# Optimization experiments

Hardware: AMD Instinct MI355X
Metric: run time of the kernel (lower is better)

Reference implementation:

```python
import jax, jax.numpy as jnp
import numpy as np

N_NODES = 100_000
N_EDGES = 1_250_000
IN_FEATS, N_HIDDEN, N_CLASSES = 64, 64, 32


def setup_inputs() -> dict:
    key = jax.random.key(0)
    ks = jax.random.split(key, 8)
    x = jax.random.normal(ks[0], (N_NODES, IN_FEATS), dtype=jnp.float32)
    src = jax.random.randint(ks[1], (N_EDGES,), 0, N_NODES, dtype=jnp.int64)
    dst = jax.random.randint(ks[2], (N_EDGES,), 0, N_NODES, dtype=jnp.int64)
    s1 = 1.0 / np.sqrt(IN_FEATS)
    s2 = 1.0 / np.sqrt(N_HIDDEN)
    W_self1 = jax.random.normal(ks[3], (IN_FEATS, N_HIDDEN), dtype=jnp.float32) * s1
    W_neigh1 = jax.random.normal(ks[4], (IN_FEATS, N_HIDDEN), dtype=jnp.float32) * s1
    b1 = jnp.zeros((N_HIDDEN,), dtype=jnp.float32)
    W_self2 = jax.random.normal(ks[5], (N_HIDDEN, N_CLASSES), dtype=jnp.float32) * s2
    W_neigh2 = jax.random.normal(ks[6], (N_HIDDEN, N_CLASSES), dtype=jnp.float32) * s2
    b2 = jnp.zeros((N_CLASSES,), dtype=jnp.float32)
    return dict(x=x, src=src, dst=dst, W_self1=W_self1, W_neigh1=W_neigh1, b1=b1,
                W_self2=W_self2, W_neigh2=W_neigh2, b2=b2)


def _sage_conv(h, src, dst, W_self, W_neigh, b):
    # mean aggregation over in-neighbors: gather src feats, segment-sum by dst
    n = h.shape[0]
    msg = h[src]  # [E, d] -- dominant memory traffic
    agg = jax.ops.segment_sum(msg, dst, num_segments=n)
    deg = jax.ops.segment_sum(jnp.ones_like(dst, dtype=h.dtype), dst, num_segments=n)
    h_neigh = agg / jnp.maximum(deg, 1.0)[:, None]  # zero-degree nodes get 0 (DGL behavior)
    return h @ W_self + h_neigh @ W_neigh + b


def reference(x, src, dst, W_self1, W_neigh1, b1, W_self2, W_neigh2, b2):
    h = _sage_conv(x, src, dst, W_self1, W_neigh1, b1)
    h = jax.nn.relu(h)
    # dropout(p=0.5) is identity in eval mode
    return _sage_conv(h, src, dst, W_self2, W_neigh2, b2)
```

## Files before the change

kernel.cpp:

```cpp
#include <hip/hip_runtime.h>
#include <hip/hip_bf16.h>


#define NF 64
#define BW 256
#define BSH 8
#define MAXB 512
#define CAPMAX 8192
#define P1_CHUNK 2048
#define H1S 68

typedef __attribute__((ext_vector_type(8))) short short8;
typedef __attribute__((ext_vector_type(8))) unsigned short ushort8v;
typedef __attribute__((ext_vector_type(4))) float floatx4;

__device__ __forceinline__ short bf16hi(float v) {
    __hip_bfloat16 h = __float2bfloat16(v);
    return *(short*)&h;
}
__device__ __forceinline__ float bf2f(short s) {
    __hip_bfloat16 h = *(__hip_bfloat16*)&s;
    return __bfloat162float(h);
}
__device__ __forceinline__ float bits2f(unsigned short u) {
    unsigned int x = ((unsigned int)u) << 16;
    union { unsigned int i; float f; } c; c.i = x; return c.f;
}


__global__ __launch_bounds__(512) void zero_kernel(int* __restrict__ g) {
    if (threadIdx.x < MAXB) g[threadIdx.x] = 0;
}


__global__ __launch_bounds__(256) void p1_bucket_kernel(const int* __restrict__ src,
                                                        const int* __restrict__ dst,
                                                        int* __restrict__ gcursor,
                                                        unsigned* __restrict__ bucket,
                                                        int E, int nbuckets) {
    __shared__ int cnt[MAXB];
    __shared__ int cbase[MAXB];
    const int beg = blockIdx.x * P1_CHUNK;
    const int end = min(E, beg + P1_CHUNK);
    for (int i = threadIdx.x; i < nbuckets; i += 256) cnt[i] = 0;
    __syncthreads();
    for (int e = beg + threadIdx.x; e < end; e += 256)
        atomicAdd(&cnt[dst[e] >> BSH], 1);
    __syncthreads();
    for (int i = threadIdx.x; i < nbuckets; i += 256) {
        int c = cnt[i];
        cbase[i] = c ? atomicAdd(&gcursor[i], c) : 0;
        cnt[i] = 0;
    }
    __syncthreads();
    for (int e = beg + threadIdx.x; e < end; e += 256) {
        int d = dst[e];
        int r = d >> BSH;
        int p = cbase[r] + atomicAdd(&cnt[r], 1);
        if (p < CAPMAX)
            bucket[(size_t)r * CAPMAX + p] = ((unsigned)src[e] << BSH) | (unsigned)(d & (BW - 1));
    }
}

__global__ __launch_bounds__(256) void p2_csr_kernel(const unsigned* __restrict__ bucket,
                                                     const int* __restrict__ gcursor,
                                                     int* __restrict__ row_start,
                                                     int* __restrict__ csr_src,
                                                     int N, int nbuckets) {
    __shared__ unsigned stage[CAPMAX];
    __shared__ int cnt[BW];
    __shared__ int excl[BW];
    const int r = blockIdx.x;
    const int tid = threadIdx.x;

    int partial = 0;
    for (int i = tid; i < r; i += 256) partial += min(gcursor[i], CAPMAX);
    excl[tid] = partial;
    __syncthreads();
    for (int off = 128; off > 0; off >>= 1) {
        if (tid < off) excl[tid] += excl[tid + off];
        __syncthreads();
    }
    const int base = excl[0];
    const int sz = min(gcursor[r], CAPMAX);
    const unsigned* bsrc = bucket + (size_t)r * CAPMAX;
    __syncthreads();

    cnt[tid] = 0;
    __syncthreads();
    for (int i = tid; i < sz; i += 256) {
        unsigned v = bsrc[i];
        stage[i] = v;
        atomicAdd(&cnt[v & (BW - 1)], 1);
    }
    __syncthreads();
    excl[tid] = cnt[tid];
    __syncthreads();
    for (int off = 1; off < BW; off <<= 1) {
        int v0 = (tid >= off) ? excl[tid - off] : 0;
        __syncthreads();
        excl[tid] += v0;
        __syncthreads();
    }
    int node = r * BW + tid;
    if (node < N) row_start[node] = base + excl[tid] - cnt[tid];
    if (r == nbuckets - 1 && tid == 0) row_start[N] = base + sz;
    __syncthreads();
    cnt[tid] = excl[tid] - cnt[tid];
    __syncthreads();
    for (int i = tid; i < sz; i += 256) {
        unsigned v = stage[i];
        int p = atomicAdd(&cnt[v & (BW - 1)], 1);
        csr_src[base + p] = (int)(v >> BSH);
    }
}


__global__ __launch_bounds__(256) void dense1_mfma_kernel(
        const float* __restrict__ X,
        const float* __restrict__ Wself,
        const float* __restrict__ Wneigh,
        const float* __restrict__ bias,
        float* __restrict__ outA,
        unsigned short* __restrict__ outB,
        int N) {
    constexpr int NT = 8, NSELF = 4, NO = 128, HALF = 64;
    __shared__ unsigned short wh[NO * 72];
    __shared__ unsigned short wl[NO * 72];
    const int tid = threadIdx.x;
    for (int i = tid; i < NO * 64; i += 256) {
        int n = i & (NO - 1), k = i / NO;
        float v = (n < HALF) ? Wself[k * HALF + n] : Wneigh[k * HALF + (n - HALF)];
        short hv = bf16hi(v);
        wh[n * 72 + k] = (unsigned short)hv;
        wl[n * 72 + k] = (unsigned short)bf16hi(v - bf2f(hv));
    }

    const int lane = tid & 63;
    const int wid  = tid >> 6;
    const int m = lane & 15, quad = lane >> 4;
    const int rowblk = blockIdx.x * 128 + wid * 32;

    floatx4 acc[2][NT];
    #pragma unroll
    for (int rt = 0; rt < 2; ++rt)
        #pragma unroll
        for (int t = 0; t < NT; ++t) acc[rt][t] = (floatx4)(0.f);

    short8 ah[2][2], al[2][2];
    #pragma unroll
    for (int rt = 0; rt < 2; ++rt) {
        int r = rowblk + rt * 16 + m;
        if (r >= N) r = N - 1;
        const float* xp = X + (size_t)r * 64 + quad * 8;
        #pragma unroll
        for (int h = 0; h < 2; ++h) {
            floatx4 f0 = *(const floatx4*)(xp + h * 32);
            floatx4 f1 = *(const floatx4*)(xp + h * 32 + 4);
            short8 hi, lo;
            #pragma unroll
            for (int j = 0; j < 4; ++j) {
                short hv = bf16hi(f0[j]);
                hi[j] = hv; lo[j] = bf16hi(f0[j] - bf2f(hv));
                short hv2 = bf16hi(f1[j]);
                hi[4 + j] = hv2; lo[4 + j] = bf16hi(f1[j] - bf2f(hv2));
            }
            ah[rt][h] = hi; al[rt][h] = lo;
        }
    }
    __syncthreads();

    #pragma unroll
    for (int t = 0; t < NT; ++t) {
        int n = t * 16 + m;
        const unsigned short* ph = wh + n * 72 + quad * 8;
        const unsigned short* pl = wl + n * 72 + quad * 8;
        #pragma unroll
        for (int h = 0; h < 2; ++h) {
            short8 bh = *(const short8*)(ph + h * 32);
            short8 bl = *(const short8*)(pl + h * 32);
            #pragma unroll
            for (int rt = 0; rt < 2; ++rt) {
                acc[rt][t] = __builtin_amdgcn_mfma_f32_16x16x32_bf16(ah[rt][h], bh, acc[rt][t], 0, 0, 0);
                acc[rt][t] = __builtin_amdgcn_mfma_f32_16x16x32_bf16(al[rt][h], bh, acc[rt][t], 0, 0, 0);
                acc[rt][t] = __builtin_amdgcn_mfma_f32_16x16x32_bf16(ah[rt][h], bl, acc[rt][t], 0, 0, 0);
            }
        }
    }

    #pragma unroll
    for (int rt = 0; rt < 2; ++rt) {
        #pragma unroll
        for (int t = 0; t < NT; ++t) {
            #pragma unroll
            for (int r4 = 0; r4 < 4; ++r4) {
                int row = rowblk + rt * 16 + quad * 4 + r4;
                if (row < N) {
                    if (t < NSELF) {
                        int col = t * 16 + m;
                        outA[(size_t)row * 64 + col] = acc[rt][t][r4] + bias[col];
                    } else {
                        int col = (t - NSELF) * 16 + m;
                        outB[(size_t)row * 64 + col] = (unsigned short)bf16hi(acc[rt][t][r4]);
                    }
                }
            }
        }
    }
}


__global__ __launch_bounds__(256) void agg64_d2_kernel(
        const unsigned short* __restrict__ t1n,
        const float* __restrict__ xs,
        const int* __restrict__ row_start,
        const int* __restrict__ csr_src,
        const float* __restrict__ Ws2,
        const float* __restrict__ Wn2,
        const float* __restrict__ b2,
        float* __restrict__ outD,
        unsigned short* __restrict__ t2n,
        int N) {
    __shared__ unsigned short w2h[64 * 72];
    __shared__ unsigned short w2l[64 * 72];
    __shared__ float h1s[16][H1S];
    const int tid = threadIdx.x;
    for (int i = tid; i < 64 * 64; i += 256) {
        int n = i & 63, k = i >> 6;
        float v = (n < 32) ? Ws2[k * 32 + n] : Wn2[k * 32 + (n - 32)];
        short hv = bf16hi(v);
        w2h[n * 72 + k] = (unsigned short)hv;
        w2l[n * 72 + k] = (unsigned short)bf16hi(v - bf2f(hv));
    }

    const int lane = tid & 63;
    const int wid  = tid >> 6;
    const int half = lane >> 5;
    const int g = (lane >> 3) & 3;
    const int c = lane & 7;
    const int nbase = blockIdx.x * 16;

    #pragma unroll
    for (int q = 0; q < 2; ++q) {
        const int ln = wid * 4 + q * 2 + half;
        const int n = nbase + ln;
        float acc[8] = {0.f, 0.f, 0.f, 0.f, 0.f, 0.f, 0.f, 0.f};
        int beg = 0, end = 0;
        if (n < N) { beg = row_start[n]; end = row_start[n + 1]; }
        for (int j = beg + g; j < end; j += 8) {
            int j2 = j + 4;
            int s0 = csr_src[j];
            ushort8v u0 = *(const ushort8v*)(t1n + (size_t)s0 * 64 + c * 8);
            if (j2 < end) {
                int s1 = csr_src[j2];
                ushort8v u1 = *(const ushort8v*)(t1n + (size_t)s1 * 64 + c * 8);
                #pragma unroll
                for (int i = 0; i < 8; ++i) acc[i] += bits2f(u0[i]) + bits2f(u1[i]);
            } else {
                #pragma unroll
                for (int i = 0; i < 8; ++i) acc[i] += bits2f(u0[i]);
            }
        }
        #pragma unroll
        for (int i = 0; i < 8; ++i) {
            float v = acc[i];
            v += __shfl_xor(v, 8);
            v += __shfl_xor(v, 16);
            acc[i] = v;
        }
        if (g == 0) {
            floatx4 h0, h1v;
            if (n < N) {
                float invd = 1.0f / fmaxf((float)(end - beg), 1.0f);
                size_t o = (size_t)n * 64 + c * 8;
                floatx4 x0 = *(const floatx4*)(xs + o);
                floatx4 x1 = *(const floatx4*)(xs + o + 4);
                #pragma unroll
                for (int i = 0; i < 4; ++i) {
                    h0[i]  = fmaxf(x0[i] + acc[i] * invd, 0.f);
                    h1v[i] = fmaxf(x1[i] + acc[4 + i] * invd, 0.f);
                }
            } else {
                h0 = (floatx4)(0.f); h1v = (floatx4)(0.f);
            }
            *(floatx4*)&h1s[ln][c * 8]     = h0;
            *(floatx4*)&h1s[ln][c * 8 + 4] = h1v;
        }
    }
    __syncthreads();

    const int m = lane & 15, quad = lane >> 4;
    short8 ah[2], al[2];
    #pragma unroll
    for (int h = 0; h < 2; ++h) {
        const float* hp = &h1s[m][quad * 8 + h * 32];
        floatx4 f0 = *(const floatx4*)hp;
        floatx4 f1 = *(const floatx4*)(hp + 4);
        short8 hi, lo;
        #pragma unroll
        for (int j = 0; j < 4; ++j) {
            short hv = bf16hi(f0[j]);
            hi[j] = hv; lo[j] = bf16hi(f0[j] - bf2f(hv));
            short hv2 = bf16hi(f1[j]);
            hi[4 + j] = hv2; lo[4 + j] = bf16hi(f1[j] - bf2f(hv2));
        }
        ah[h] = hi; al[h] = lo;
    }
    floatx4 acc2 = (floatx4)(0.f);
    const int coln = wid * 16 + m;
    const unsigned short* ph = w2h + coln * 72 + quad * 8;
    const unsigned short* pl = w2l + coln * 72 + quad * 8;
    #pragma unroll
    for (int h = 0; h < 2; ++h) {
        short8 bh = *(const short8*)(ph + h * 32);
        short8 bl = *(const short8*)(pl + h * 32);
        acc2 = __builtin_amdgcn_mfma_f32_16x16x32_bf16(ah[h], bh, acc2, 0, 0, 0);
        acc2 = __builtin_amdgcn_mfma_f32_16x16x32_bf16(al[h], bh, acc2, 0, 0, 0);
        acc2 = __builtin_amdgcn_mfma_f32_16x16x32_bf16(ah[h], bl, acc2, 0, 0, 0);
    }
    #pragma unroll
    for (int r4 = 0; r4 < 4; ++r4) {
        int node = nbase + quad * 4 + r4;
        if (node < N) {
            if (coln < 32) outD[(size_t)node * 32 + coln] = acc2[r4] + b2[coln];
            else t2n[(size_t)node * 32 + (coln - 32)] = (unsigned short)bf16hi(acc2[r4]);
        }
    }
}


__global__ __launch_bounds__(256) void agg32_kernel(float* io,
                                                    const unsigned short* __restrict__ t2n,
                                                    const int* __restrict__ row_start,
                                                    const int* __restrict__ csr_src, int N) {
    int n = (blockIdx.x * blockDim.x + threadIdx.x) >> 6;
    if (n >= N) return;
    int lane = threadIdx.x & 63;
    int g = lane >> 2, c = lane & 3;
    int beg = row_start[n], end = row_start[n + 1];
    float acc[8] = {0.f, 0.f, 0.f, 0.f, 0.f, 0.f, 0.f, 0.f};
    for (int j = beg + g; j < end; j += 32) {
        int j2 = j + 16;
        int s0 = csr_src[j];
        ushort8v u0 = *(const ushort8v*)(t2n + (size_t)s0 * 32 + c * 8);
        if (j2 < end) {
            int s1 = csr_src[j2];
            ushort8v u1 = *(const ushort8v*)(t2n + (size_t)s1 * 32 + c * 8);
            #pragma unroll
            for (int i = 0; i < 8; ++i) acc[i] += bits2f(u0[i]) + bits2f(u1[i]);
        } else {
            #pragma unroll
            for (int i = 0; i < 8; ++i) acc[i] += bits2f(u0[i]);
        }
    }
    #pragma unroll
    for (int i = 0; i < 8; ++i) {
        float v = acc[i];
        v += __shfl_xor(v, 4);
        v += __shfl_xor(v, 8);
        v += __shfl_xor(v, 16);
        v += __shfl_xor(v, 32);
        acc[i] = v;
    }
    if (g == 0) {
        float inv = 1.0f / fmaxf((float)(end - beg), 1.0f);
        size_t o = (size_t)n * 32 + c * 8;
        floatx4 s0 = *(const floatx4*)(io + o);
        floatx4 s1 = *(const floatx4*)(io + o + 4);
        floatx4 r0, r1;
        #pragma unroll
        for (int i = 0; i < 4; ++i) {
            r0[i] = s0[i] + acc[i] * inv;
            r1[i] = s1[i] + acc[4 + i] * inv;
        }
        *(floatx4*)(io + o) = r0;
        *(floatx4*)(io + o + 4) = r1;
    }
}


__global__ __launch_bounds__(256) void deg_kernel(const int* __restrict__ dst,
                                                  float* __restrict__ deg, int E) {
    int e = blockIdx.x * blockDim.x + threadIdx.x;
    if (e < E) atomicAdd(&deg[dst[e]], 1.0f);
}

__global__ __launch_bounds__(256) void agg_atomic_kernel(const float* __restrict__ feats,
                                                         const int* __restrict__ src,
                                                         const int* __restrict__ dst,
                                                         float* __restrict__ agg, int E) {
    int tid = blockIdx.x * blockDim.x + threadIdx.x;
    if (tid >= E * NF) return;
    int e = tid >> 6, f = tid & 63;
    atomicAdd(&agg[(size_t)dst[e] * NF + f], feats[(size_t)src[e] * NF + f]);
}

__global__ __launch_bounds__(256) void layer1_fb_kernel(const float* __restrict__ x,
                                                        const float* __restrict__ agg,
                                                        const float* __restrict__ deg,
                                                        const float* __restrict__ Wself,
                                                        const float* __restrict__ Wneigh,
                                                        const float* __restrict__ b,
                                                        float* __restrict__ h1, int N) {
    int tid = blockIdx.x * blockDim.x + threadIdx.x;
    if (tid >= N * NF) return;
    int n = tid >> 6, c = tid & 63;
    float inv = 1.0f / fmaxf(deg[n], 1.0f);
    const float* xrow = x + (size_t)n * NF;
    const float* arow = agg + (size_t)n * NF;
    float acc = b[c];
    #pragma unroll
    for (int k = 0; k < NF; ++k) {
        acc += xrow[k] * Wself[k * NF + c];
        acc += (arow[k] * inv) * Wneigh[k * NF + c];
    }
    h1[tid] = fmaxf(acc, 0.f);
}

__global__ __launch_bounds__(256) void layer2_fb_kernel(const float* __restrict__ h1,
                                                        const float* __restrict__ agg,
                                                        const float* __restrict__ deg,
                                                        const float* __restrict__ Wself,
                                                        const float* __restrict__ Wneigh,
                                                        const float* __restrict__ b,
                                                        float* __restrict__ out, int N) {
    int tid = blockIdx.x * blockDim.x + threadIdx.x;
    if (tid >= N * 32) return;
    int n = tid >> 5, c = tid & 31;
    float inv = 1.0f / fmaxf(deg[n], 1.0f);
    const float* hrow = h1 + (size_t)n * NF;
    const float* arow = agg + (size_t)n * NF;
    float acc = b[c];
    #pragma unroll
    for (int k = 0; k < NF; ++k) {
        acc += hrow[k] * Wself[k * 32 + c];
        acc += (arow[k] * inv) * Wneigh[k * 32 + c];
    }
    out[tid] = acc;
}


extern "C" void kernel_launch(void* const* d_in, const int* in_sizes, int n_in,
                              void* d_out, int out_size, void* d_ws, size_t ws_size,
                              hipStream_t stream) {
    const float* x        = (const float*)d_in[0];
    const int*   src      = (const int*)d_in[1];
    const int*   dst      = (const int*)d_in[2];
    const float* W_self1  = (const float*)d_in[3];
    const float* W_neigh1 = (const float*)d_in[4];
    const float* b1       = (const float*)d_in[5];
    const float* W_self2  = (const float*)d_in[6];
    const float* W_neigh2 = (const float*)d_in[7];
    const float* b2       = (const float*)d_in[8];
    float* out = (float*)d_out;

    const int N = in_sizes[0] / NF;
    const int E = in_sizes[1];
    const int nbuckets = (N + BW - 1) / BW;

    const size_t rsPad = ((size_t)N + 8) & ~7ull;
    int* gcursor   = (int*)d_ws;
    int* row_start = gcursor + MAXB;
    int* csr_src   = row_start + rsPad;
    uintptr_t pa = (uintptr_t)(csr_src + (((size_t)E + 7) & ~7ull));
    pa = (pa + 127) & ~(uintptr_t)127;
    float* bufA = (float*)pa;
    unsigned* bucket = (unsigned*)bufA;
    unsigned short* t1n = (unsigned short*)(bufA + (size_t)N * NF);
    unsigned short* t2n = t1n + (size_t)N * NF;
    size_t need = (size_t)((char*)(t2n + (size_t)N * 32) - (char*)d_ws);

    bool fast = ws_size >= need
             && nbuckets <= MAXB
             && (size_t)nbuckets * CAPMAX <= (size_t)N * NF
             && (size_t)E * 2 / (size_t)nbuckets <= CAPMAX
             && N < (1 << 24)
             && out_size >= N * 32;

    if (fast) {
        zero_kernel<<<1, 512, 0, stream>>>(gcursor);
        p1_bucket_kernel<<<(E + P1_CHUNK - 1) / P1_CHUNK, 256, 0, stream>>>(
            src, dst, gcursor, bucket, E, nbuckets);
        p2_csr_kernel<<<nbuckets, 256, 0, stream>>>(bucket, gcursor,
                                                    row_start, csr_src, N, nbuckets);
        int dblocks = (N + 127) / 128;
        dense1_mfma_kernel<<<dblocks, 256, 0, stream>>>(x, W_self1, W_neigh1, b1,
                                                        bufA, t1n, N);
        agg64_d2_kernel<<<(N + 15) / 16, 256, 0, stream>>>(
            t1n, bufA, row_start, csr_src, W_self2, W_neigh2, b2, out, t2n, N);
        agg32_kernel<<<(N * 64 + 255) / 256, 256, 0, stream>>>(out, t2n,
                                                               row_start, csr_src, N);
    } else {
        float* deg = (float*)d_ws;
        float* agg = deg + N;
        float* h1  = agg + (size_t)N * NF;
        hipMemsetAsync(deg, 0, (size_t)(N + (size_t)N * NF) * sizeof(float), stream);
        deg_kernel<<<(E + 255) / 256, 256, 0, stream>>>(dst, deg, E);
        int at = E * NF;
        agg_atomic_kernel<<<(at + 255) / 256, 256, 0, stream>>>(x, src, dst, agg, E);
        layer1_fb_kernel<<<(N * NF + 255) / 256, 256, 0, stream>>>(x, agg, deg, W_self1,
                                                                   W_neigh1, b1, h1, N);
        hipMemsetAsync(agg, 0, (size_t)N * NF * sizeof(float), stream);
        agg_atomic_kernel<<<(at + 255) / 256, 256, 0, stream>>>(h1, src, dst, agg, E);
        layer2_fb_kernel<<<(N * 32 + 255) / 256, 256, 0, stream>>>(h1, agg, deg, W_self2,
                                                                   W_neigh2, b2, out, N);
    }
}
```

Baseline: 226.5 us.

## Fuse edge bucketing and layer-1 dense GEMM into one launch

Merges the edge-bucketing pass and the first dense MFMA transform into a single kernel, with block IDs past the dense range running the bucketing work. The two independent stages can then share the GPU concurrently and one launch is saved. To avoid clobbering bufA, the bucket scratch moves to a separate workspace region after t2n when space allows, otherwise it falls back to sequential launches. The shared-memory footprint is now the larger of the two stage needs, which may lower occupancy for the bucketing blocks.

Result: faster. 215.3 us (median of 2 runs) (-4.9%).

```diff
diff --git a/kernel.cpp b/kernel.cpp
--- a/kernel.cpp
+++ b/kernel.cpp
@@ -33,90 +33,10 @@
 }
 
 
-__global__ __launch_bounds__(256) void p1_bucket_kernel(const int* __restrict__ src,
-                                                        const int* __restrict__ dst,
-                                                        int* __restrict__ gcursor,
-                                                        unsigned* __restrict__ bucket,
-                                                        int E, int nbuckets) {
-    __shared__ int cnt[MAXB];
-    __shared__ int cbase[MAXB];
-    const int beg = blockIdx.x * P1_CHUNK;
-    const int end = min(E, beg + P1_CHUNK);
-    for (int i = threadIdx.x; i < nbuckets; i += 256) cnt[i] = 0;
-    __syncthreads();
-    for (int e = beg + threadIdx.x; e < end; e += 256)
-        atomicAdd(&cnt[dst[e] >> BSH], 1);
-    __syncthreads();
-    for (int i = threadIdx.x; i < nbuckets; i += 256) {
-        int c = cnt[i];
-        cbase[i] = c ? atomicAdd(&gcursor[i], c) : 0;
-        cnt[i] = 0;
-    }
-    __syncthreads();
-    for (int e = beg + threadIdx.x; e < end; e += 256) {
-        int d = dst[e];
-        int r = d >> BSH;
-        int p = cbase[r] + atomicAdd(&cnt[r], 1);
-        if (p < CAPMAX)
-            bucket[(size_t)r * CAPMAX + p] = ((unsigned)src[e] << BSH) | (unsigned)(d & (BW - 1));
-    }
-}
-
-__global__ __launch_bounds__(256) void p2_csr_kernel(const unsigned* __restrict__ bucket,
-                                                     const int* __restrict__ gcursor,
-                                                     int* __restrict__ row_start,
-                                                     int* __restrict__ csr_src,
-                                                     int N, int nbuckets) {
-    __shared__ unsigned stage[CAPMAX];
-    __shared__ int cnt[BW];
-    __shared__ int excl[BW];
-    const int r = blockIdx.x;
-    const int tid = threadIdx.x;
-
-    int partial = 0;
-    for (int i = tid; i < r; i += 256) partial += min(gcursor[i], CAPMAX);
-    excl[tid] = partial;
-    __syncthreads();
-    for (int off = 128; off > 0; off >>= 1) {
-        if (tid < off) excl[tid] += excl[tid + off];
-        __syncthreads();
-    }
-    const int base = excl[0];
-    const int sz = min(gcursor[r], CAPMAX);
-    const unsigned* bsrc = bucket + (size_t)r * CAPMAX;
-    __syncthreads();
-
-    cnt[tid] = 0;
-    __syncthreads();
-    for (int i = tid; i < sz; i += 256) {
-        unsigned v = bsrc[i];
-        stage[i] = v;
-        atomicAdd(&cnt[v & (BW - 1)], 1);
-    }
-    __syncthreads();
-    excl[tid] = cnt[tid];
-    __syncthreads();
-    for (int off = 1; off < BW; off <<= 1) {
-        int v0 = (tid >= off) ? excl[tid - off] : 0;
-        __syncthreads();
-        excl[tid] += v0;
-        __syncthreads();
-    }
-    int node = r * BW + tid;
-    if (node < N) row_start[node] = base + excl[tid] - cnt[tid];
-    if (r == nbuckets - 1 && tid == 0) row_start[N] = base + sz;
-    __syncthreads();
-    cnt[tid] = excl[tid] - cnt[tid];
-    __syncthreads();
-    for (int i = tid; i < sz; i += 256) {
-        unsigned v = stage[i];
-        int p = atomicAdd(&cnt[v & (BW - 1)], 1);
-        csr_src[base + p] = (int)(v >> BSH);
-    }
-}
-
-
-__global__ __launch_bounds__(256) void dense1_mfma_kernel(
+__global__ __launch_bounds__(256) void p1_dense1_kernel(
+        const int* __restrict__ src, const int* __restrict__ dst,
+        int* __restrict__ gcursor, unsigned* __restrict__ bucket,
+        int E, int nbuckets, int dblocks,
         const float* __restrict__ X,
         const float* __restrict__ Wself,
         const float* __restrict__ Wneigh,
@@ -124,10 +44,39 @@
         float* __restrict__ outA,
         unsigned short* __restrict__ outB,
         int N) {
+    __shared__ int smem_i[9216];
+    const int tid = threadIdx.x;
+
+    if ((int)blockIdx.x >= dblocks) {
+        int* cnt   = smem_i;
+        int* cbase = smem_i + MAXB;
+        const int bid = blockIdx.x - dblocks;
+        const int beg = bid * P1_CHUNK;
+        const int end = min(E, beg + P1_CHUNK);
+        for (int i = tid; i < nbuckets; i += 256) cnt[i] = 0;
+        __syncthreads();
+        for (int e = beg + tid; e < end; e += 256)
+            atomicAdd(&cnt[dst[e] >> BSH], 1);
+        __syncthreads();
+        for (int i = tid; i < nbuckets; i += 256) {
+            int c = cnt[i];
+            cbase[i] = c ? atomicAdd(&gcursor[i], c) : 0;
+            cnt[i] = 0;
+        }
+        __syncthreads();
+        for (int e = beg + tid; e < end; e += 256) {
+            int d = dst[e];
+            int r = d >> BSH;
+            int p = cbase[r] + atomicAdd(&cnt[r], 1);
+            if (p < CAPMAX)
+                bucket[(size_t)r * CAPMAX + p] = ((unsigned)src[e] << BSH) | (unsigned)(d & (BW - 1));
+        }
+        return;
+    }
+
     constexpr int NT = 8, NSELF = 4, NO = 128, HALF = 64;
-    __shared__ unsigned short wh[NO * 72];
-    __shared__ unsigned short wl[NO * 72];
-    const int tid = threadIdx.x;
+    unsigned short* wh = (unsigned short*)smem_i;
+    unsigned short* wl = wh + NO * 72;
     for (int i = tid; i < NO * 64; i += 256) {
         int n = i & (NO - 1), k = i / NO;
         float v = (n < HALF) ? Wself[k * HALF + n] : Wneigh[k * HALF + (n - HALF)];
@@ -206,6 +155,60 @@
                 }
             }
         }
+    }
+}
+
+
+__global__ __launch_bounds__(256) void p2_csr_kernel(const unsigned* __restrict__ bucket,
+                                                     const int* __restrict__ gcursor,
+                                                     int* __restrict__ row_start,
+                                                     int* __restrict__ csr_src,
+                                                     int N, int nbuckets) {
+    __shared__ unsigned stage[CAPMAX];
+    __shared__ int cnt[BW];
+    __shared__ int excl[BW];
+    const int r = blockIdx.x;
+    const int tid = threadIdx.x;
+
+    int partial = 0;
+    for (int i = tid; i < r; i += 256) partial += min(gcursor[i], CAPMAX);
+    excl[tid] = partial;
+    __syncthreads();
+    for (int off = 128; off > 0; off >>= 1) {
+        if (tid < off) excl[tid] += excl[tid + off];
+        __syncthreads();
+    }
+    const int base = excl[0];
+    const int sz = min(gcursor[r], CAPMAX);
+    const unsigned* bsrc = bucket + (size_t)r * CAPMAX;
+    __syncthreads();
+
+    cnt[tid] = 0;
+    __syncthreads();
+    for (int i = tid; i < sz; i += 256) {
+        unsigned v = bsrc[i];
+        stage[i] = v;
+        atomicAdd(&cnt[v & (BW - 1)], 1);
+    }
+    __syncthreads();
+    excl[tid] = cnt[tid];
+    __syncthreads();
+    for (int off = 1; off < BW; off <<= 1) {
+        int v0 = (tid >= off) ? excl[tid - off] : 0;
+        __syncthreads();
+        excl[tid] += v0;
+        __syncthreads();
+    }
+    int node = r * BW + tid;
+    if (node < N) row_start[node] = base + excl[tid] - cnt[tid];
+    if (r == nbuckets - 1 && tid == 0) row_start[N] = base + sz;
+    __syncthreads();
+    cnt[tid] = excl[tid] - cnt[tid];
+    __syncthreads();
+    for (int i = tid; i < sz; i += 256) {
+        unsigned v = stage[i];
+        int p = atomicAdd(&cnt[v & (BW - 1)], 1);
+        csr_src[base + p] = (int)(v >> BSH);
     }
 }
 
@@ -479,13 +482,26 @@
 
     if (fast) {
         zero_kernel<<<1, 512, 0, stream>>>(gcursor);
-        p1_bucket_kernel<<<(E + P1_CHUNK - 1) / P1_CHUNK, 256, 0, stream>>>(
-            src, dst, gcursor, bucket, E, nbuckets);
-        p2_csr_kernel<<<nbuckets, 256, 0, stream>>>(bucket, gcursor,
-                                                    row_start, csr_src, N, nbuckets);
-        int dblocks = (N + 127) / 128;
-        dense1_mfma_kernel<<<dblocks, 256, 0, stream>>>(x, W_self1, W_neigh1, b1,
-                                                        bufA, t1n, N);
+        int dblocks  = (N + 127) / 128;
+        int p1blocks = (E + P1_CHUNK - 1) / P1_CHUNK;
+        unsigned* bucket2 = (unsigned*)(t2n + (((size_t)N * 32 + 63) & ~63ull));
+        size_t need2 = (size_t)((char*)(bucket2 + (size_t)nbuckets * CAPMAX) - (char*)d_ws);
+        if (ws_size >= need2) {
+            p1_dense1_kernel<<<dblocks + p1blocks, 256, 0, stream>>>(
+                src, dst, gcursor, bucket2, E, nbuckets, dblocks,
+                x, W_self1, W_neigh1, b1, bufA, t1n, N);
+            p2_csr_kernel<<<nbuckets, 256, 0, stream>>>(bucket2, gcursor,
+                                                        row_start, csr_src, N, nbuckets);
+        } else {
+            p1_dense1_kernel<<<p1blocks, 256, 0, stream>>>(
+                src, dst, gcursor, bucket, E, nbuckets, 0,
+                x, W_self1, W_neigh1, b1, bufA, t1n, N);
+            p2_csr_kernel<<<nbuckets, 256, 0, stream>>>(bucket, gcursor,
+                                                        row_start, csr_src, N, nbuckets);
+            p1_dense1_kernel<<<dblocks, 256, 0, stream>>>(
+                src, dst, gcursor, bucket, E, nbuckets, dblocks,
+                x, W_self1, W_neigh1, b1, bufA, t1n, N);
+        }
         agg64_d2_kernel<<<(N + 15) / 16, 256, 0, stream>>>(
             t1n, bufA, row_start, csr_src, W_self2, W_neigh2, b2, out, t2n, N);
         agg32_kernel<<<(N * 64 + 255) / 256, 256, 0, stream>>>(out, t2n,
```
